# Kernel optimization log

Measured on AMD Instinct MI355X. Metric: run time of the kernel, lower is better.

The kernel has to match this reference:

```python
import math
import jax, jax.numpy as jnp
import numpy as np

B, C, N, CUT = 64, 3, 512, 4
T_TEMP = 0.01


def setup_inputs() -> dict:
    key = jax.random.key(0)
    k1, k2, k3 = jax.random.split(key, 3)
    x = jax.random.normal(k1, (B, C, N, N), dtype=jnp.float32)
    F_x = jax.random.normal(k2, (B, CUT, CUT), dtype=jnp.float32)
    F_y = jax.random.normal(k3, (B, CUT, CUT), dtype=jnp.float32)
    return {"x": x, "F_x": F_x, "F_y": F_y}


def _scalar_field(n, m, F):
    # low-frequency sinusoidal field: [B, m, m] coeffs -> [B, n, n] field
    dtype = F.dtype
    xs = jnp.linspace(0.0, 1.0, n, dtype=dtype)
    k = jnp.arange(1, m + 1, dtype=dtype)
    i, j = jnp.meshgrid(k, k, indexing="ij")
    r = jnp.sqrt(i * i + j * j)
    e = (r < m + 0.5).astype(dtype) / r            # radial cutoff envelope [m, m]
    s = jnp.sin(jnp.pi * xs[:, None] * k[None, :])  # [n, m]
    return jnp.einsum("bij,xi,yj->byx", F * e[None], s, s)


def reference(x, F_x, F_y):
    Bn, Cc, n, m = x.shape
    cut = F_x.shape[-1]
    dtype = x.dtype
    u = _scalar_field(n, cut, F_x)
    v = _scalar_field(n, cut, F_y)
    # typical_displacement(1, cut, n) = n * (pi * log(cut))**0.5 / 2
    typ = n * (math.pi * math.log(cut)) ** 0.5 / 2.0
    scale = (T_TEMP / typ ** 2) ** 0.5 * n
    dx = scale * u  # [B, n, n]
    dy = scale * v
    yy, xx = jnp.meshgrid(jnp.arange(n, dtype=dtype), jnp.arange(m, dtype=dtype), indexing="ij")
    xn = jnp.clip(xx[None] - dx, 0.0, m - 1)  # [B, n, n]
    yn = jnp.clip(yy[None] - dy, 0.0, n - 1)
    xf = jnp.floor(xn).astype(jnp.int32)
    yf = jnp.floor(yn).astype(jnp.int32)
    xc = jnp.ceil(xn).astype(jnp.int32)
    yc = jnp.ceil(yn).astype(jnp.int32)
    xv = xn - xf  # bilinear weights [B, n, n]
    yv = yn - yf

    def gather(img, yi, xi):
        # img: [C, n, n], yi/xi: [n, n] -> [C, n, n]
        return img[:, yi, xi]

    G = jax.vmap(gather)  # over batch
    w00 = ((1 - yv) * (1 - xv))[:, None]
    w01 = ((1 - yv) * xv)[:, None]
    w10 = (yv * (1 - xv))[:, None]
    w11 = (yv * xv)[:, None]
    out = (w00 * G(x, yf, xf) + w01 * G(x, yf, xc)
           + w10 * G(x, yc, xf) + w11 * G(x, yc, xc))
    return out
```

## Files before the change

kernel.cpp:

```cpp
#include <hip/hip_runtime.h>
#include <math.h>

#define NN 512
#define NC 3

__device__ __constant__ float d_env[16] = {
    0.70710678f, 0.44721360f, 0.31622777f, 0.24253563f,
    0.44721360f, 0.35355339f, 0.27735010f, 0.22360680f,
    0.31622777f, 0.27735010f, 0.23570226f, 0.00000000f,
    0.24253563f, 0.22360680f, 0.00000000f, 0.00000000f
};

__global__ __launch_bounds__(256) void sine_table_kernel(float* __restrict__ ws) {
    const int t = blockIdx.x * 256 + threadIdx.x;
    const int j = t & 3;
    const int p = t >> 2;
    ws[t] = sinf((float)M_PI * (float)p * (1.0f / 511.0f) * (float)(j + 1));
}

__global__ __launch_bounds__(256) void diffeo_kernel(
    const float* __restrict__ xin,
    const float* __restrict__ Fx,
    const float* __restrict__ Fy,
    float* __restrict__ out,
    const float* __restrict__ ws,
    float scale)
{
    const int tid = threadIdx.x;
    const int bid = blockIdx.x;
    const int row = ((bid & 7) << 12) | (bid >> 3);
    const int b = row >> 9;
    const int y = row & (NN - 1);

    const float4 sy = *(const float4*)(ws + y * 4);
    const float syv[4] = { sy.x, sy.y, sy.z, sy.w };

    const float* fx = Fx + b * 16;
    const float* fy = Fy + b * 16;
    float cu[4], cv[4];
#pragma unroll
    for (int i = 0; i < 4; ++i) {
        float su = 0.0f, sv = 0.0f;
#pragma unroll
        for (int j = 0; j < 4; ++j) {
            const float w = d_env[i * 4 + j] * syv[j];
            su += fx[i * 4 + j] * w;
            sv += fy[i * 4 + j] * w;
        }
        cu[i] = scale * su;
        cv[i] = scale * sv;
    }

    const float* __restrict__ base  = xin + (size_t)b * NC * NN * NN;
    float* __restrict__       obase = out + (size_t)b * NC * NN * NN + (size_t)y * NN;
    const float yr = (float)y;

#pragma unroll
    for (int p = 0; p < 2; ++p) {
        const int xx = tid + (p << 8);

        const float4 sx = *(const float4*)(ws + xx * 4);
        const float du = sx.x * cu[0] + sx.y * cu[1] + sx.z * cu[2] + sx.w * cu[3];
        const float dv = sx.x * cv[0] + sx.y * cv[1] + sx.z * cv[2] + sx.w * cv[3];

        const float xn = fminf(fmaxf((float)xx - du, 0.0f), 511.0f);
        const float yn = fminf(fmaxf(yr - dv, 0.0f), 511.0f);
        const float xff = floorf(xn), yff = floorf(yn);
        const int xf = (int)xff, yf = (int)yff;
        const int xc = min(xf + 1, NN - 1);
        const int yc = min(yf + 1, NN - 1);
        const float xv = xn - xff, yv = yn - yff;

        const int o00 = yf * NN + xf;
        const int o01 = yf * NN + xc;
        const int o10 = yc * NN + xf;
        const int o11 = yc * NN + xc;

#pragma unroll
        for (int c = 0; c < NC; ++c) {
            const float* img = base + c * NN * NN;
            const float v00 = img[o00];
            const float v01 = img[o01];
            const float v10 = img[o10];
            const float v11 = img[o11];
            const float top = v00 + xv * (v01 - v00);
            const float bot = v10 + xv * (v11 - v10);
            obase[c * NN * NN + xx] = top + yv * (bot - top);
        }
    }
}

extern "C" void kernel_launch(void* const* d_in, const int* in_sizes, int n_in,
                              void* d_out, int out_size, void* d_ws, size_t ws_size,
                              hipStream_t stream) {
    const float* x  = (const float*)d_in[0];
    const float* Fx = (const float*)d_in[1];
    const float* Fy = (const float*)d_in[2];
    float* out = (float*)d_out;
    float* ws  = (float*)d_ws;

    const double typ = 512.0 * sqrt(M_PI * log(4.0)) / 2.0;
    const float scale = (float)(sqrt(0.01 / (typ * typ)) * 512.0);

    sine_table_kernel<<<8, 256, 0, stream>>>(ws);
    diffeo_kernel<<<64 * 512, 256, 0, stream>>>(x, Fx, Fy, out, ws, scale);
}
```

Measured before the change: 349.1 us.

## Stage 8-row input tiles with halo in LDS via global_load_lds for bilinear gather

Each block now handles 8 output rows of one batch image. It first copies the matching 12 input rows (2-row halo on each side) for all three channels, plus the sine table, into shared memory using async global-to-LDS loads. Bilinear samples are then read from LDS, with a fallback to global gathers when the displaced row falls outside the staged window. Outputs use nontemporal stores, and the launch switches to 512-thread blocks. The aim is to replace scattered uncached global gathers with coalesced row loads, at the cost of about 80 KB of LDS per block, which limits occupancy.

```diff
diff --git a/kernel.cpp b/kernel.cpp
--- a/kernel.cpp
+++ b/kernel.cpp
@@ -18,7 +18,12 @@
     ws[t] = sinf((float)M_PI * (float)p * (1.0f / 511.0f) * (float)(j + 1));
 }
 
-__global__ __launch_bounds__(256) void diffeo_kernel(
+#define GLOAD_LDS(g, l)                                                        \
+    __builtin_amdgcn_global_load_lds(                                          \
+        (const __attribute__((address_space(1))) void*)(g),                    \
+        (__attribute__((address_space(3))) void*)(l), 16, 0, 0)
+
+__global__ __launch_bounds__(512, 4) void diffeo_kernel(
     const float* __restrict__ xin,
     const float* __restrict__ Fx,
     const float* __restrict__ Fy,
@@ -28,15 +33,39 @@
 {
     const int tid = threadIdx.x;
     const int bid = blockIdx.x;
-    const int row = ((bid & 7) << 12) | (bid >> 3);
-    const int b = row >> 9;
-    const int y = row & (NN - 1);
+    const int g  = ((bid & 7) << 9) | (bid >> 3);
+    const int b  = g >> 6;
+    const int y0 = (g & 63) << 3;
+    const int lo = y0 - 2;
 
-    const float4 sy = *(const float4*)(ws + y * 4);
-    const float syv[4] = { sy.x, sy.y, sy.z, sy.w };
+    __shared__ float smem[20480];
+    const float* __restrict__ base = xin + (size_t)b * NC * NN * NN;
+
+    GLOAD_LDS(ws + (tid << 2), smem + 18432 + (tid << 2));
+
+#pragma unroll
+    for (int k = 0; k < 9; ++k) {
+        const int f   = tid + (k << 9);
+        const int ch  = (f >= 3072) ? 2 : ((f >= 1536) ? 1 : 0);
+        const int rem = f - ch * 1536;
+        const int srow = rem >> 7;
+        const int seg  = rem & 127;
+        const int row  = min(max(lo + srow, 0), NN - 1);
+        GLOAD_LDS(base + ((ch << 18) | (row << 9) | (seg << 2)),
+                  smem + (f << 2));
+    }
+
+    const int y  = y0 + (tid >> 6);
+    const int xb = tid & 63;
 
     const float* fx = Fx + b * 16;
     const float* fy = Fy + b * 16;
+
+    __syncthreads();
+
+    const float4 sy = *(const float4*)(smem + 18432 + (y << 2));
+    const float syv[4] = { sy.x, sy.y, sy.z, sy.w };
+
     float cu[4], cv[4];
 #pragma unroll
     for (int i = 0; i < 4; ++i) {
@@ -51,15 +80,14 @@
         cv[i] = scale * sv;
     }
 
-    const float* __restrict__ base  = xin + (size_t)b * NC * NN * NN;
-    float* __restrict__       obase = out + (size_t)b * NC * NN * NN + (size_t)y * NN;
+    float* __restrict__ obase = out + (size_t)b * NC * NN * NN + (size_t)y * NN;
     const float yr = (float)y;
 
-#pragma unroll
-    for (int p = 0; p < 2; ++p) {
-        const int xx = tid + (p << 8);
+#pragma unroll 4
+    for (int k = 0; k < 8; ++k) {
+        const int xx = xb | (k << 6);
 
-        const float4 sx = *(const float4*)(ws + xx * 4);
+        const float4 sx = *(const float4*)(smem + 18432 + (xx << 2));
         const float du = sx.x * cu[0] + sx.y * cu[1] + sx.z * cu[2] + sx.w * cu[3];
         const float dv = sx.x * cv[0] + sx.y * cv[1] + sx.z * cv[2] + sx.w * cv[3];
 
@@ -67,26 +95,47 @@
         const float yn = fminf(fmaxf(yr - dv, 0.0f), 511.0f);
         const float xff = floorf(xn), yff = floorf(yn);
         const int xf = (int)xff, yf = (int)yff;
-        const int xc = min(xf + 1, NN - 1);
-        const int yc = min(yf + 1, NN - 1);
         const float xv = xn - xff, yv = yn - yff;
 
-        const int o00 = yf * NN + xf;
-        const int o01 = yf * NN + xc;
-        const int o10 = yc * NN + xf;
-        const int o11 = yc * NN + xc;
+        float o0, o1, o2;
+        if (yf >= lo && yf <= lo + 10) {
+            const float* t0 = smem + (((yf - lo) << 9) + xf);
+            const float* t1 = t0 + 512;
+#pragma unroll
+            for (int c = 0; c < NC; ++c) {
+                const float v00 = t0[c * 6144 + 0];
+                const float v01 = t0[c * 6144 + 1];
+                const float v10 = t1[c * 6144 + 0];
+                const float v11 = t1[c * 6144 + 1];
+                const float top = v00 + xv * (v01 - v00);
+                const float bot = v10 + xv * (v11 - v10);
+                const float r = top + yv * (bot - top);
+                if (c == 0) o0 = r; else if (c == 1) o1 = r; else o2 = r;
+            }
+        } else {
+            const int xc = min(xf + 1, NN - 1);
+            const int yc = min(yf + 1, NN - 1);
+            const int o00 = yf * NN + xf;
+            const int o01 = yf * NN + xc;
+            const int o10 = yc * NN + xf;
+            const int o11 = yc * NN + xc;
+#pragma unroll
+            for (int c = 0; c < NC; ++c) {
+                const float* img = base + c * NN * NN;
+                const float v00 = img[o00];
+                const float v01 = img[o01];
+                const float v10 = img[o10];
+                const float v11 = img[o11];
+                const float top = v00 + xv * (v01 - v00);
+                const float bot = v10 + xv * (v11 - v10);
+                const float r = top + yv * (bot - top);
+                if (c == 0) o0 = r; else if (c == 1) o1 = r; else o2 = r;
+            }
+        }
 
-#pragma unroll
-        for (int c = 0; c < NC; ++c) {
-            const float* img = base + c * NN * NN;
-            const float v00 = img[o00];
-            const float v01 = img[o01];
-            const float v10 = img[o10];
-            const float v11 = img[o11];
-            const float top = v00 + xv * (v01 - v00);
-            const float bot = v10 + xv * (v11 - v10);
-            obase[c * NN * NN + xx] = top + yv * (bot - top);
-        }
+        __builtin_nontemporal_store(o0, obase + 0 * NN * NN + xx);
+        __builtin_nontemporal_store(o1, obase + 1 * NN * NN + xx);
+        __builtin_nontemporal_store(o2, obase + 2 * NN * NN + xx);
     }
 }
 
@@ -103,5 +152,5 @@
     const float scale = (float)(sqrt(0.01 / (typ * typ)) * 512.0);
 
     sine_table_kernel<<<8, 256, 0, stream>>>(ws);
-    diffeo_kernel<<<64 * 512, 256, 0, stream>>>(x, Fx, Fy, out, ws, scale);
+    diffeo_kernel<<<64 * 64, 512, 0, stream>>>(x, Fx, Fy, out, ws, scale);
 }
```

Measured after the change: 337.4 us. 1.03x faster.

## Stream source rows through an LDS ring buffer with async global-to-LDS loads

Applied to the files above, without the earlier changes.

Replaces the one-block-per-row launch with 256 persistent 1024-thread blocks. Each block handles 128 rows of one image and prefetches upcoming source rows into a 16-row LDS ring using global_load_lds, so bilinear taps that fall inside the window are read from LDS, with a fallback to global memory for larger displacements. Per-row displacement coefficients are precomputed once into shared memory, and outputs use nontemporal stores. The aim is to cut redundant global gather traffic and overlap loads with compute. In exchange it brings a much lower block count (fewer blocks than needed to fill every CU well), a barrier per iteration, and delicate vmcnt-based synchronisation.

```diff
diff --git a/kernel.cpp b/kernel.cpp
--- a/kernel.cpp
+++ b/kernel.cpp
@@ -3,6 +3,9 @@
 
 #define NN 512
 #define NC 3
+#define RING 16
+#define SLOTF (NC * NN)
+#define TBL   (RING * SLOTF)
 
 __device__ __constant__ float d_env[16] = {
     0.70710678f, 0.44721360f, 0.31622777f, 0.24253563f,
@@ -18,7 +21,12 @@
     ws[t] = sinf((float)M_PI * (float)p * (1.0f / 511.0f) * (float)(j + 1));
 }
 
-__global__ __launch_bounds__(256) void diffeo_kernel(
+#define GLOAD_LDS(g, l)                                                        \
+    __builtin_amdgcn_global_load_lds(                                          \
+        (const __attribute__((address_space(1))) void*)(g),                    \
+        (__attribute__((address_space(3))) void*)(l), 16, 0, 0)
+
+__global__ __launch_bounds__(1024) void diffeo_kernel(
     const float* __restrict__ xin,
     const float* __restrict__ Fx,
     const float* __restrict__ Fy,
@@ -26,66 +34,132 @@
     const float* __restrict__ ws,
     float scale)
 {
+    __shared__ float smem[TBL + 128 * 8];
+
     const int tid = threadIdx.x;
     const int bid = blockIdx.x;
-    const int row = ((bid & 7) << 12) | (bid >> 3);
-    const int b = row >> 9;
-    const int y = row & (NN - 1);
+    const int g  = ((bid & 7) << 5) | (bid >> 3);
+    const int b  = g >> 2;
+    const int ys = (g & 3) << 7;
 
-    const float4 sy = *(const float4*)(ws + y * 4);
-    const float syv[4] = { sy.x, sy.y, sy.z, sy.w };
+    const float* __restrict__ base = xin + (size_t)b * NC * NN * NN;
 
-    const float* fx = Fx + b * 16;
-    const float* fy = Fy + b * 16;
-    float cu[4], cv[4];
 #pragma unroll
-    for (int i = 0; i < 4; ++i) {
-        float su = 0.0f, sv = 0.0f;
-#pragma unroll
-        for (int j = 0; j < 4; ++j) {
-            const float w = d_env[i * 4 + j] * syv[j];
-            su += fx[i * 4 + j] * w;
-            sv += fy[i * 4 + j] * w;
+    for (int k = 0; k < 3; ++k) {
+        const int f = tid + (k << 10);
+        if (f < 2304) {
+            const int rc = f >> 7;
+            const int ch = (rc >= 12) ? 2 : ((rc >= 6) ? 1 : 0);
+            const int ro = rc - ch * 6;
+            const int lr = ys - 1 + ro;
+            const int sr = max(lr, 0);
+            GLOAD_LDS(base + ((ch << 18) | (sr << 9)) + ((f & 127) << 2),
+                      smem + (lr & (RING - 1)) * SLOTF + ch * NN + ((f & 127) << 2));
         }
-        cu[i] = scale * su;
-        cv[i] = scale * sv;
     }
 
-    const float* __restrict__ base  = xin + (size_t)b * NC * NN * NN;
-    float* __restrict__       obase = out + (size_t)b * NC * NN * NN + (size_t)y * NN;
-    const float yr = (float)y;
+    {
+        const int ri = tid >> 3, comp = tid & 7, i = comp & 3;
+        const float* Fp = ((comp & 4) ? Fy : Fx) + b * 16 + i * 4;
+        const float4 sy = *(const float4*)(ws + ((ys + ri) << 2));
+        smem[TBL + (ri << 3) + comp] = scale *
+            (Fp[0] * d_env[i * 4 + 0] * sy.x + Fp[1] * d_env[i * 4 + 1] * sy.y +
+             Fp[2] * d_env[i * 4 + 2] * sy.z + Fp[3] * d_env[i * 4 + 3] * sy.w);
+    }
+
+    const int xb   = tid & 255;
+    const int wrow = tid >> 8;
+    const float4 sxA = *(const float4*)(ws + (xb << 2));
+    const float4 sxB = *(const float4*)(ws + ((xb + 256) << 2));
+
+    float* __restrict__ ob = out + (size_t)b * NC * NN * NN;
+
+    __syncthreads();
+
+    for (int it = 0; it < 32; ++it) {
+        const int y0 = ys + (it << 2);
+
+        if (it < 31) {
+            {
+                const int f  = tid;
+                const int rc = f >> 7;
+                const int ch = rc >> 2, ro = rc & 3;
+                const int lr = y0 + 5 + ro;
+                const int sr = min(lr, NN - 1);
+                GLOAD_LDS(base + ((ch << 18) | (sr << 9)) + ((f & 127) << 2),
+                          smem + (lr & (RING - 1)) * SLOTF + ch * NN + ((f & 127) << 2));
+            }
+            if (tid < 512) {
+                const int f  = tid + 1024;
+                const int ro = (f >> 7) & 3;
+                const int lr = y0 + 5 + ro;
+                const int sr = min(lr, NN - 1);
+                GLOAD_LDS(base + ((2 << 18) | (sr << 9)) + ((f & 127) << 2),
+                          smem + (lr & (RING - 1)) * SLOTF + 2 * NN + ((f & 127) << 2));
+            }
+        }
+
+        asm volatile("s_waitcnt vmcnt(6)" ::: "memory");
+        __builtin_amdgcn_s_barrier();
+        asm volatile("" ::: "memory");
+
+        const int y  = y0 + wrow;
+        const int ri = (it << 2) + wrow;
+        const float4 cu = *(const float4*)(smem + TBL + (ri << 3));
+        const float4 cv = *(const float4*)(smem + TBL + (ri << 3) + 4);
+        const float yr = (float)y;
+        float* __restrict__ orow = ob + (size_t)y * NN;
 
 #pragma unroll
-    for (int p = 0; p < 2; ++p) {
-        const int xx = tid + (p << 8);
+        for (int k = 0; k < 2; ++k) {
+            const int xx = xb + (k << 8);
+            const float4 sx = k ? sxB : sxA;
+            const float du = sx.x * cu.x + sx.y * cu.y + sx.z * cu.z + sx.w * cu.w;
+            const float dv = sx.x * cv.x + sx.y * cv.y + sx.z * cv.z + sx.w * cv.w;
 
-        const float4 sx = *(const float4*)(ws + xx * 4);
-        const float du = sx.x * cu[0] + sx.y * cu[1] + sx.z * cu[2] + sx.w * cu[3];
-        const float dv = sx.x * cv[0] + sx.y * cv[1] + sx.z * cv[2] + sx.w * cv[3];
+            const float xn = fminf(fmaxf((float)xx - du, 0.0f), 511.0f);
+            const float yn = fminf(fmaxf(yr - dv, 0.0f), 511.0f);
+            const int xf = min((int)floorf(xn), NN - 2);
+            const int yf = min((int)floorf(yn), NN - 2);
+            const float xv = xn - (float)xf;
+            const float yv = yn - (float)yf;
 
-        const float xn = fminf(fmaxf((float)xx - du, 0.0f), 511.0f);
-        const float yn = fminf(fmaxf(yr - dv, 0.0f), 511.0f);
-        const float xff = floorf(xn), yff = floorf(yn);
-        const int xf = (int)xff, yf = (int)yff;
-        const int xc = min(xf + 1, NN - 1);
-        const int yc = min(yf + 1, NN - 1);
-        const float xv = xn - xff, yv = yn - yff;
+            float o0, o1, o2;
+            if ((unsigned)(yf - (y0 - 1)) <= 4u) {
+                const float* t0 = smem + (yf & (RING - 1)) * SLOTF + xf;
+                const float* t1 = smem + ((yf + 1) & (RING - 1)) * SLOTF + xf;
+#pragma unroll
+                for (int c = 0; c < NC; ++c) {
+                    const float v00 = t0[c * NN];
+                    const float v01 = t0[c * NN + 1];
+                    const float v10 = t1[c * NN];
+                    const float v11 = t1[c * NN + 1];
+                    const float top = v00 + xv * (v01 - v00);
+                    const float bot = v10 + xv * (v11 - v10);
+                    const float r = top + yv * (bot - top);
+                    if (c == 0) o0 = r; else if (c == 1) o1 = r; else o2 = r;
+                }
+            } else {
+                const int xc = xf + 1, yc = yf + 1;
+                const int o00 = yf * NN + xf, o01 = yf * NN + xc;
+                const int o10 = yc * NN + xf, o11 = yc * NN + xc;
+#pragma unroll
+                for (int c = 0; c < NC; ++c) {
+                    const float* img = base + c * NN * NN;
+                    const float v00 = img[o00];
+                    const float v01 = img[o01];
+                    const float v10 = img[o10];
+                    const float v11 = img[o11];
+                    const float top = v00 + xv * (v01 - v00);
+                    const float bot = v10 + xv * (v11 - v10);
+                    const float r = top + yv * (bot - top);
+                    if (c == 0) o0 = r; else if (c == 1) o1 = r; else o2 = r;
+                }
+            }
 
-        const int o00 = yf * NN + xf;
-        const int o01 = yf * NN + xc;
-        const int o10 = yc * NN + xf;
-        const int o11 = yc * NN + xc;
-
-#pragma unroll
-        for (int c = 0; c < NC; ++c) {
-            const float* img = base + c * NN * NN;
-            const float v00 = img[o00];
-            const float v01 = img[o01];
-            const float v10 = img[o10];
-            const float v11 = img[o11];
-            const float top = v00 + xv * (v01 - v00);
-            const float bot = v10 + xv * (v11 - v10);
-            obase[c * NN * NN + xx] = top + yv * (bot - top);
+            __builtin_nontemporal_store(o0, orow + 0 * NN * NN + xx);
+            __builtin_nontemporal_store(o1, orow + 1 * NN * NN + xx);
+            __builtin_nontemporal_store(o2, orow + 2 * NN * NN + xx);
         }
     }
 }
@@ -103,5 +177,5 @@
     const float scale = (float)(sqrt(0.01 / (typ * typ)) * 512.0);
 
     sine_table_kernel<<<8, 256, 0, stream>>>(ws);
-    diffeo_kernel<<<64 * 512, 256, 0, stream>>>(x, Fx, Fy, out, ws, scale);
+    diffeo_kernel<<<256, 1024, 0, stream>>>(x, Fx, Fy, out, ws, scale);
 }
```

Result: no change. 349.4 us (+0.1%).
